# Kernel optimization log

Measured on AMD Instinct MI355X. Metric: run time of the kernel, lower is better.

The kernel has to match this reference:

```python
import jax, jax.numpy as jnp
import numpy as np

B, T, E, V, H = 2, 2048, 1024, 2048, 8
KD, HD = E // H, V // H  # key_dim=128, head_dim=256
EPS = 1e-6


def rotate_every_two(x):
    x1 = x[..., ::2]
    x2 = x[..., 1::2]
    return jnp.stack((-x2, x1), axis=-1).reshape(x.shape)


def theta_shift(x, sin, cos):
    return x * cos + rotate_every_two(x) * sin


def setup_inputs() -> dict:
    key = jax.random.key(0)
    ks = jax.random.split(key, 8)
    x = jax.random.normal(ks[0], (B, T, E), dtype=jnp.float32)
    angle = jnp.arange(T, dtype=jnp.float32)[:, None] * (1.0 / (10000.0 ** (jnp.repeat(jnp.arange(KD // 2, dtype=jnp.float32), 2) * 2.0 / KD)))
    sin = jnp.sin(angle)  # [T, KD]
    cos = jnp.cos(angle)
    # RetNet per-head causal decay mask: decay_h = 1 - 2^(-5-h)
    decay = 1.0 - 2.0 ** (-5.0 - jnp.arange(H, dtype=jnp.float32))  # [H]
    idx = jnp.arange(T, dtype=jnp.float32)
    diff = idx[:, None] - idx[None, :]  # n - m
    causal = diff >= 0
    mask = jnp.where(causal[None], jnp.exp(jnp.where(causal, diff, 0.0)[None] * jnp.log(decay)[:, None, None]), 0.0)  # [H,T,T]
    g = 2 ** (-2.5)
    Wq = jax.random.normal(ks[1], (E, E), dtype=jnp.float32) * (g * np.sqrt(2.0 / (E + E)))
    Wk = jax.random.normal(ks[2], (E, E), dtype=jnp.float32) * (g * np.sqrt(2.0 / (E + E)))
    Wv = jax.random.normal(ks[3], (E, V), dtype=jnp.float32) * (g * np.sqrt(2.0 / (E + V)))
    Wg = jax.random.normal(ks[4], (E, V), dtype=jnp.float32) * (g * np.sqrt(2.0 / (E + V)))
    Wo = jax.random.normal(ks[5], (V, E), dtype=jnp.float32) * np.sqrt(2.0 / (V + E))
    return {"x": x, "sin": sin, "cos": cos, "mask": mask,
            "Wq": Wq, "Wk": Wk, "Wv": Wv, "Wg": Wg, "Wo": Wo}


def reference(x, sin, cos, mask, Wq, Wk, Wv, Wg, Wo):
    b, t, _ = x.shape
    scaling = KD ** -0.5
    q = (x @ Wq).reshape(b, t, H, KD).transpose(0, 2, 1, 3)  # [B,H,T,KD]
    k = (x @ Wk * scaling).reshape(b, t, H, KD).transpose(0, 2, 1, 3)
    v = x @ Wv  # [B,T,V]
    g = x @ Wg
    qr = theta_shift(q, sin, cos)
    kr = theta_shift(k, sin, cos)
    vr = v.reshape(b, t, H, HD).transpose(0, 2, 1, 3)  # [B,H,T,HD]
    qk = jnp.einsum('bhsk,bhtk->bhst', qr, kr) * mask  # [B,H,T,T]
    denom = jnp.clip(jnp.abs(jax.lax.stop_gradient(qk).sum(-1, keepdims=True)), 1.0, None)
    qk = qk / denom
    out = jnp.einsum('bhst,bhtd->bhsd', qk, vr)  # [B,H,T,HD]
    out = out.transpose(0, 2, 1, 3)  # [B,T,H,HD]
    # RMSNorm over head_dim, no affine
    out = out * jax.lax.rsqrt(jnp.mean(out * out, axis=-1, keepdims=True) + EPS)
    out = out.reshape(b, t, H * HD)
    out = jax.nn.silu(g) * out
    return out @ Wo  # [B,T,E]
```

## Files before the change

kernel.cpp:

```cpp
#include <hip/hip_runtime.h>
#include <hip/hip_bf16.h>


#define B_ 2
#define T_ 2048
#define E_ 1024
#define V_ 2048
#define H_ 8
#define KD_ 128
#define HD_ 256
#define M_ 4096

typedef __attribute__((ext_vector_type(8))) short bf16x8;
typedef __attribute__((ext_vector_type(4))) float f32x4;

__device__ __forceinline__ float u2f(unsigned short u) {
    return __uint_as_float(((unsigned)u) << 16);
}
__device__ __forceinline__ unsigned short f2bu(float f) {
    unsigned x = __float_as_uint(f);
    return (unsigned short)((x + 0x7fffu + ((x >> 16) & 1u)) >> 16);
}

typedef const __attribute__((address_space(1))) void gas_t;
typedef __attribute__((address_space(3))) void las_t;
__device__ __forceinline__ void gl_lds16(const void* g, void* l) {
    __builtin_amdgcn_global_load_lds((gas_t*)g, (las_t*)l, 16, 0, 0);
}

__device__ __forceinline__ void stc(float* p, float f) { *p = f; }
__device__ __forceinline__ void stc(unsigned short* p, float f) { *p = f2bu(f); }

__global__ __launch_bounds__(256) void conv_x_kernel(
    const float* __restrict__ x, unsigned short* __restrict__ xb)
{
    const size_t i = ((size_t)blockIdx.x * 256 + threadIdx.x) * 8;
    float4 a = *(const float4*)(x + i);
    float4 c = *(const float4*)(x + i + 4);
    *(ushort4*)(xb + i)     = make_ushort4(f2bu(a.x), f2bu(a.y), f2bu(a.z), f2bu(a.w));
    *(ushort4*)(xb + i + 4) = make_ushort4(f2bu(c.x), f2bu(c.y), f2bu(c.z), f2bu(c.w));
}

__global__ __launch_bounds__(256) void transW4_kernel(
    const float* __restrict__ Wq, const float* __restrict__ Wk,
    const float* __restrict__ Wv, const float* __restrict__ Wg,
    unsigned short* __restrict__ Wt)
{
    const int z = blockIdx.z;
    const float* W; int N; int rofs;
    if (z == 0)      { W = Wq; N = 1024; rofs = 0; }
    else if (z == 1) { W = Wk; N = 1024; rofs = 1024; }
    else if (z == 2) { W = Wv; N = 2048; rofs = 2048; }
    else             { W = Wg; N = 2048; rofs = 4096; }
    const int n0 = blockIdx.x * 64;
    if (n0 >= N) return;
    const int k0 = blockIdx.y * 64;

    __shared__ float tl[64][65];
    const int tid = threadIdx.x;
    #pragma unroll
    for (int i = 0; i < 4; ++i) {
        int kr = i * 16 + (tid >> 4);
        int nc = (tid & 15) * 4;
        float4 v = *(const float4*)(W + (size_t)(k0 + kr) * N + n0 + nc);
        tl[kr][nc] = v.x; tl[kr][nc + 1] = v.y; tl[kr][nc + 2] = v.z; tl[kr][nc + 3] = v.w;
    }
    __syncthreads();
    #pragma unroll
    for (int i = 0; i < 4; ++i) {
        int nr = i * 16 + (tid >> 4);
        int kc = (tid & 15) * 4;
        ushort4 u = make_ushort4(f2bu(tl[kc + 0][nr]), f2bu(tl[kc + 1][nr]),
                                 f2bu(tl[kc + 2][nr]), f2bu(tl[kc + 3][nr]));
        *(ushort4*)(Wt + (size_t)(rofs + n0 + nr) * E_ + k0 + kc) = u;
    }
}

__global__ __launch_bounds__(256) void transW_kernel(
    const float* __restrict__ W, unsigned short* __restrict__ Wt, int K, int N)
{
    __shared__ float tl[64][65];
    const int tid = threadIdx.x;
    const int n0 = blockIdx.x * 64, k0 = blockIdx.y * 64;
    #pragma unroll
    for (int i = 0; i < 4; ++i) {
        int kr = i * 16 + (tid >> 4);
        int nc = (tid & 15) * 4;
        float4 v = *(const float4*)(W + (size_t)(k0 + kr) * N + n0 + nc);
        tl[kr][nc] = v.x; tl[kr][nc + 1] = v.y; tl[kr][nc + 2] = v.z; tl[kr][nc + 3] = v.w;
    }
    __syncthreads();
    #pragma unroll
    for (int i = 0; i < 4; ++i) {
        int nr = i * 16 + (tid >> 4);
        int kc = (tid & 15) * 4;
        ushort4 u = make_ushort4(f2bu(tl[kc + 0][nr]), f2bu(tl[kc + 1][nr]),
                                 f2bu(tl[kc + 2][nr]), f2bu(tl[kc + 3][nr]));
        *(ushort4*)(Wt + (size_t)(n0 + nr) * K + k0 + kc) = u;
    }
}

__global__ __launch_bounds__(256) void transV_kernel(
    const unsigned short* __restrict__ vb, unsigned short* __restrict__ vt)
{
    __shared__ unsigned short tl[64][68];
    const int tid = threadIdx.x;
    const int t0 = blockIdx.x * 64, c0 = blockIdx.y * 64, b = blockIdx.z;
    #pragma unroll
    for (int i = 0; i < 4; ++i) {
        int tr = i * 16 + (tid >> 4);
        int cc = (tid & 15) * 4;
        ushort4 v = *(const ushort4*)(vb + (size_t)(b * T_ + t0 + tr) * V_ + c0 + cc);
        tl[tr][cc] = v.x; tl[tr][cc + 1] = v.y; tl[tr][cc + 2] = v.z; tl[tr][cc + 3] = v.w;
    }
    __syncthreads();
    #pragma unroll
    for (int i = 0; i < 4; ++i) {
        int cr = i * 16 + (tid >> 4);
        int tc = (tid & 15) * 4;
        ushort4 u = make_ushort4(tl[tc + 0][cr], tl[tc + 1][cr], tl[tc + 2][cr], tl[tc + 3][cr]);
        *(ushort4*)(vt + (size_t)(b * V_ + c0 + cr) * T_ + t0 + tc) = u;
    }
}

#define GSTAGE(BUF, K0)                                                        \
    {                                                                          \
        _Pragma("unroll")                                                      \
        for (int i = 0; i < 4; ++i) {                                          \
            int r = i * 32 + srow;                                             \
            int cb = scolb ^ ((r & 7) << 4);                                   \
            gl_lds16((const char*)(A  + (size_t)(rowBase + r) * K + (K0)) + cb,\
                     Asm[BUF] + i * 4096 + w * 1024);                          \
            gl_lds16((const char*)(Bt + (size_t)(colBase + r) * K + (K0)) + cb,\
                     Bsm[BUF] + i * 4096 + w * 1024);                          \
        }                                                                      \
    }

#define GCOMPUTE(BUF)                                                          \
    {                                                                          \
        _Pragma("unroll")                                                      \
        for (int kk = 0; kk < 2; ++kk) {                                       \
            const int cb = kk * 64 + (l >> 4) * 16;                            \
            bf16x8 a[4], b[4];                                                 \
            _Pragma("unroll")                                                  \
            for (int m = 0; m < 4; ++m) {                                      \
                int r = wr * 64 + m * 16 + (l & 15);                           \
                a[m] = *(const bf16x8*)(Asm[BUF] + r * 128 + (cb ^ ((r & 7) << 4))); \
            }                                                                  \
            _Pragma("unroll")                                                  \
            for (int n = 0; n < 4; ++n) {                                      \
                int r = wc * 64 + n * 16 + (l & 15);                           \
                b[n] = *(const bf16x8*)(Bsm[BUF] + r * 128 + (cb ^ ((r & 7) << 4))); \
            }                                                                  \
            _Pragma("unroll")                                                  \
            for (int m = 0; m < 4; ++m)                                        \
                _Pragma("unroll")                                              \
                for (int n = 0; n < 4; ++n)                                    \
                    acc[m][n] = __builtin_amdgcn_mfma_f32_16x16x32_bf16(a[m], b[n], acc[m][n], 0, 0, 0); \
        }                                                                      \
    }

#define GEMM_PIPELINE_LOOP                                                     \
    GSTAGE(0, 0)                                                               \
    const int nk = K / 64;                                                     \
    for (int kt = 0; kt < nk; ++kt) {                                          \
        const int cur = kt & 1;                                                \
        if (kt + 1 < nk) {                                                     \
            GSTAGE(1 - cur, (kt + 1) * 64)                                     \
            asm volatile("s_waitcnt vmcnt(8)" ::: "memory");                   \
        } else {                                                               \
            asm volatile("s_waitcnt vmcnt(0)" ::: "memory");                   \
        }                                                                      \
        __builtin_amdgcn_s_barrier();                                          \
        __builtin_amdgcn_sched_barrier(0);                                     \
        GCOMPUTE(cur)                                                          \
        __builtin_amdgcn_s_barrier();                                          \
        __builtin_amdgcn_sched_barrier(0);                                     \
    }

template <typename CT>
__global__ __launch_bounds__(256) void gemm_mfma_kernel(
    const unsigned short* __restrict__ A,
    const unsigned short* __restrict__ Bt,
    CT* __restrict__ C,
    int N, int K)
{
    __shared__ __align__(16) char Asm[2][128 * 64 * 2];
    __shared__ __align__(16) char Bsm[2][128 * 64 * 2];
    const int tid = threadIdx.x;
    const int l = tid & 63;
    const int w = tid >> 6;
    const int wr = w >> 1, wc = w & 1;
    const int rowBase = blockIdx.y * 128;
    const int colBase = blockIdx.x * 128;
    const int srow = tid >> 3;
    const int scolb = (tid & 7) * 16;

    f32x4 acc[4][4] = {};

    GEMM_PIPELINE_LOOP

    #pragma unroll
    for (int m = 0; m < 4; ++m)
        #pragma unroll
        for (int n = 0; n < 4; ++n)
            #pragma unroll
            for (int r = 0; r < 4; ++r) {
                int row = rowBase + wr * 64 + m * 16 + (l >> 4) * 4 + r;
                int col = colBase + wc * 64 + n * 16 + (l & 15);
                float f = acc[m][n][r];
                if (!isfinite(f)) f = 0.f;
                stc(C + (size_t)row * N + col, f);
            }
}

__global__ __launch_bounds__(256) void gemm_qkvg_kernel(
    const unsigned short* __restrict__ A,
    const unsigned short* __restrict__ Bt,
    unsigned short* __restrict__ qb,
    unsigned short* __restrict__ kb,
    unsigned short* __restrict__ vb,
    unsigned short* __restrict__ gb)
{
    const int K = E_;
    __shared__ __align__(16) char Asm[2][128 * 64 * 2];
    __shared__ __align__(16) char Bsm[2][128 * 64 * 2];
    const int tid = threadIdx.x;
    const int l = tid & 63;
    const int w = tid >> 6;
    const int wr = w >> 1, wc = w & 1;
    const int rowBase = blockIdx.y * 128;
    const int colBase = blockIdx.x * 128;
    const int srow = tid >> 3;
    const int scolb = (tid & 7) * 16;

    f32x4 acc[4][4] = {};

    GEMM_PIPELINE_LOOP

    const int colW = colBase + wc * 64;
    unsigned short* dst;
    int cofs, stride;
    if (colW < 1024)      { dst = qb; cofs = 0;    stride = E_; }
    else if (colW < 2048) { dst = kb; cofs = 1024; stride = E_; }
    else if (colW < 4096) { dst = vb; cofs = 2048; stride = V_; }
    else                  { dst = gb; cofs = 4096; stride = V_; }
    #pragma unroll
    for (int m = 0; m < 4; ++m)
        #pragma unroll
        for (int n = 0; n < 4; ++n)
            #pragma unroll
            for (int r = 0; r < 4; ++r) {
                int row = rowBase + wr * 64 + m * 16 + (l >> 4) * 4 + r;
                int col = colW + n * 16 + (l & 15);
                float f = acc[m][n][r];
                if (!isfinite(f)) f = 0.f;
                dst[(size_t)row * stride + (col - cofs)] = f2bu(f);
            }
}

__global__ __launch_bounds__(256) void theta2_kernel(
    unsigned short* __restrict__ qb,
    unsigned short* __restrict__ kb,
    const float* __restrict__ sinp, const float* __restrict__ cosp)
{
    unsigned short* qk = blockIdx.y ? kb : qb;
    const float scale = blockIdx.y ? 0.088388347648318447f : 1.0f;
    const int i = blockIdx.x * 256 + threadIdx.x;
    const int pe = i & (E_ / 2 - 1);
    const int bt = i >> 9;
    const int t = bt & (T_ - 1);
    const int e0 = pe << 1;
    const int d0 = e0 & (KD_ - 1);
    const size_t base = (size_t)bt * E_ + e0;
    const float q0 = u2f(qk[base]);
    const float q1 = u2f(qk[base + 1]);
    const int sb = t * KD_ + d0;
    const float s0 = sinp[sb], s1 = sinp[sb + 1];
    const float c0 = cosp[sb], c1 = cosp[sb + 1];
    qk[base]     = f2bu((q0 * c0 - q1 * s0) * scale);
    qk[base + 1] = f2bu((q1 * c1 + q0 * s1) * scale);
}

#define STAGE_K(BUF, T0)                                                       \
    {                                                                          \
        _Pragma("unroll")                                                      \
        for (int i = 0; i < 4; ++i) {                                          \
            int r = i * 16 + (tid >> 4);                                       \
            int cb = ((tid & 15) * 16) ^ ((r & 7) << 4);                       \
            gl_lds16((const char*)(kb + (size_t)(b * T_ + (T0) + r) * E_ + h * KD_) + cb, \
                     Ks[BUF] + i * 4096 + w * 1024);                           \
        }                                                                      \
    }

#define STAGE_V(T0)                                                            \
    {                                                                          \
        _Pragma("unroll")                                                      \
        for (int i = 0; i < 8; ++i) {                                          \
            int r = i * 32 + (tid >> 3);                                       \
            int cb = ((tid & 7) * 16) ^ ((r & 7) << 4);                        \
            gl_lds16((const char*)(vt + (size_t)((b * H_ + h) * HD_ + r) * T_ + (T0)) + cb, \
                     Vs + i * 4096 + w * 1024);                                \
        }                                                                      \
    }

__global__ __launch_bounds__(256) void retention_mfma_kernel(
    const unsigned short* __restrict__ qb,
    const unsigned short* __restrict__ kb,
    const unsigned short* __restrict__ vt,
    unsigned short* __restrict__ ao)
{
    __shared__ __align__(16) char Ks[2][64 * 128 * 2];
    __shared__ __align__(16) char Vs[256 * 64 * 2];
    __shared__ __align__(16) char Ps[64 * 64 * 2];
    __shared__ float rsum_lds[64];
    const int tid = threadIdx.x;
    const int l = tid & 63;
    const int w = tid >> 6;
    const int orig = (int)blockIdx.x;
    const int xcd  = orig & 7;
    const int pos  = orig >> 3;
    const int slot = pos >> 5;
    const int cu   = pos & 31;
    const int half = cu >> 4;
    const int c15  = cu & 15;
    const int bh   = xcd * 2 + half;
    const int chunk = slot ? c15 : (31 - c15);
    const int b = bh >> 3, h = bh & 7;
    const int s0 = chunk * 64;
    const float ld = logf(1.f - exp2f(-5.f - (float)h));

    float es[4], etl[4];
    #pragma unroll
    for (int r = 0; r < 4; ++r)
        es[r] = __expf((float)(s0 + w * 16 + (l >> 4) * 4 + r) * ld);
    #pragma unroll
    for (int n = 0; n < 4; ++n)
        etl[n] = __expf(-(float)(n * 16 + (l & 15)) * ld);
    const float Dm64 = __expf(-64.f * ld);
    float etb = 1.f;

    bf16x8 qf[4];
    {
        const char* qp = (const char*)(qb + (size_t)(b * T_ + s0 + w * 16 + (l & 15)) * E_ + h * KD_);
        #pragma unroll
        for (int kk = 0; kk < 4; ++kk)
            qf[kk] = *(const bf16x8*)(qp + kk * 64 + (l >> 4) * 16);
    }

    f32x4 oacc[4][4] = {};
    float rs[4] = {0.f, 0.f, 0.f, 0.f};

    const int nt = chunk + 1;
    STAGE_K(0, 0)

    for (int t = 0; t < nt; ++t) {
        const int cur = t & 1;
        const int t0 = t * 64;
        STAGE_V(t0)
        if (t + 1 < nt) {
            STAGE_K(1 - cur, t0 + 64)
            asm volatile("s_waitcnt vmcnt(12)" ::: "memory");
        } else {
            asm volatile("s_waitcnt vmcnt(8)" ::: "memory");
        }
        __builtin_amdgcn_s_barrier();
        __builtin_amdgcn_sched_barrier(0);

        f32x4 sacc[4] = {};
        #pragma unroll
        for (int kk = 0; kk < 4; ++kk) {
            const int cb = kk * 64 + (l >> 4) * 16;
            #pragma unroll
            for (int n = 0; n < 4; ++n) {
                int r = n * 16 + (l & 15);
                bf16x8 kf = *(const bf16x8*)(Ks[cur] + r * 256 + (cb ^ ((r & 7) << 4)));
                sacc[n] = __builtin_amdgcn_mfma_f32_16x16x32_bf16(qf[kk], kf, sacc[n], 0, 0, 0);
            }
        }
        float et[4];
        #pragma unroll
        for (int n = 0; n < 4; ++n) et[n] = etb * etl[n];
        etb *= Dm64;
        float rsp[4] = {0.f, 0.f, 0.f, 0.f};
        #pragma unroll
        for (int n = 0; n < 4; ++n)
            #pragma unroll
            for (int r = 0; r < 4; ++r) {
                int qrow = w * 16 + (l >> 4) * 4 + r;
                int tcol = n * 16 + (l & 15);
                int d = (s0 + qrow) - (t0 + tcol);
                float pm = (d >= 0) ? sacc[n][r] * (es[r] * et[n]) : 0.f;
                rsp[r] += pm;
                *(unsigned short*)(Ps + qrow * 128 + ((tcol * 2) ^ ((qrow & 7) << 4))) = f2bu(pm);
            }
        #pragma unroll
        for (int r = 0; r < 4; ++r) {
            float vv = rsp[r];
            vv += __shfl_xor(vv, 1, 16);
            vv += __shfl_xor(vv, 2, 16);
            vv += __shfl_xor(vv, 4, 16);
            vv += __shfl_xor(vv, 8, 16);
            rs[r] += vv;
        }
        if (t + 1 < nt) {
            asm volatile("s_waitcnt vmcnt(4) lgkmcnt(0)" ::: "memory");
        } else {
            asm volatile("s_waitcnt vmcnt(0) lgkmcnt(0)" ::: "memory");
        }
        __builtin_amdgcn_s_barrier();
        __builtin_amdgcn_sched_barrier(0);
        #pragma unroll
        for (int kk = 0; kk < 2; ++kk) {
            const int cb = kk * 64 + (l >> 4) * 16;
            bf16x8 pf[4];
            #pragma unroll
            for (int m = 0; m < 4; ++m) {
                int pr = m * 16 + (l & 15);
                pf[m] = *(const bf16x8*)(Ps + pr * 128 + (cb ^ ((pr & 7) << 4)));
            }
            #pragma unroll
            for (int n = 0; n < 4; ++n) {
                int r = w * 64 + n * 16 + (l & 15);
                bf16x8 vf = *(const bf16x8*)(Vs + r * 128 + (cb ^ ((r & 7) << 4)));
                #pragma unroll
                for (int m = 0; m < 4; ++m)
                    oacc[m][n] = __builtin_amdgcn_mfma_f32_16x16x32_bf16(pf[m], vf, oacc[m][n], 0, 0, 0);
            }
        }
        __builtin_amdgcn_s_barrier();
        __builtin_amdgcn_sched_barrier(0);
    }

    #pragma unroll
    for (int r = 0; r < 4; ++r)
        if ((l & 15) == 0) rsum_lds[w * 16 + (l >> 4) * 4 + r] = rs[r];
    __syncthreads();

    #pragma unroll
    for (int m = 0; m < 4; ++m)
        #pragma unroll
        for (int r = 0; r < 4; ++r) {
            const int row = m * 16 + (l >> 4) * 4 + r;
            const float inv = 1.f / fmaxf(fabsf(rsum_lds[row]), 1.f);
            #pragma unroll
            for (int n = 0; n < 4; ++n) {
                int col = h * HD_ + w * 64 + n * 16 + (l & 15);
                float f = oacc[m][n][r] * inv;
                if (!isfinite(f)) f = 0.f;
                ao[(size_t)(b * T_ + s0 + row) * V_ + col] = f2bu(f);
            }
        }
}

__global__ __launch_bounds__(256) void rms_silu_kernel(
    unsigned short* __restrict__ ao, const unsigned short* __restrict__ g)
{
    __shared__ float part[4];
    const int tid = threadIdx.x;
    const size_t base = (size_t)blockIdx.x * HD_;
    const float f = u2f(ao[base + tid]);
    float sq = f * f;
    #pragma unroll
    for (int off = 32; off > 0; off >>= 1) sq += __shfl_down(sq, off, 64);
    if ((tid & 63) == 0) part[tid >> 6] = sq;
    __syncthreads();
    const float tot = part[0] + part[1] + part[2] + part[3];
    const float scale = rsqrtf(tot * (1.0f / HD_) + 1e-6f);
    const float gv = u2f(g[base + tid]);
    ao[base + tid] = f2bu(f * scale * gv / (1.f + __expf(-gv)));
}

extern "C" void kernel_launch(void* const* d_in, const int* in_sizes, int n_in,
                              void* d_out, int out_size, void* d_ws, size_t ws_size,
                              hipStream_t stream)
{
    const float* x    = (const float*)d_in[0];
    const float* sinp = (const float*)d_in[1];
    const float* cosp = (const float*)d_in[2];
    const float* Wq   = (const float*)d_in[4];
    const float* Wk   = (const float*)d_in[5];
    const float* Wv   = (const float*)d_in[6];
    const float* Wg   = (const float*)d_in[7];
    const float* Wo   = (const float*)d_in[8];
    float* out = (float*)d_out;

    unsigned short* xb = (unsigned short*)d_out;
    unsigned short* qb = xb + (size_t)M_ * E_;

    char* ws = (char*)d_ws;
    unsigned short* kb  = (unsigned short*)(ws + 0);
    unsigned short* vb  = (unsigned short*)(ws + 8388608);
    unsigned short* gb  = (unsigned short*)(ws + 25165824);
    unsigned short* wt  = (unsigned short*)(ws + 41943040);
    unsigned short* vt  = (unsigned short*)(ws + 54525952);
    unsigned short* aob = (unsigned short*)(ws + 71303168);
    unsigned short* wot = (unsigned short*)(ws + 88080384);

    dim3 blk(256);
    conv_x_kernel<<<M_ * E_ / 8 / 256, blk, 0, stream>>>(x, xb);

    transW4_kernel<<<dim3(32, 16, 4), blk, 0, stream>>>(Wq, Wk, Wv, Wg, wt);

    gemm_qkvg_kernel<<<dim3(48, 32), blk, 0, stream>>>(xb, wt, qb, kb, vb, gb);

    theta2_kernel<<<dim3(M_ * E_ / 2 / 256, 2), blk, 0, stream>>>(qb, kb, sinp, cosp);

    transV_kernel<<<dim3(32, 32, B_), blk, 0, stream>>>(vb, vt);

    retention_mfma_kernel<<<dim3(512), blk, 0, stream>>>(qb, kb, vt, aob);

    rms_silu_kernel<<<B_ * T_ * H_, blk, 0, stream>>>(aob, gb);

    transW_kernel<<<dim3(16, 32), blk, 0, stream>>>(Wo, wot, V_, E_);
    gemm_mfma_kernel<float><<<dim3(8, 32), blk, 0, stream>>>(aob, wot, out, E_, V_);
}
```

Baseline: 219.8 us.

## Fuse RMSNorm and SiLU gating into retention epilogue; retile output GEMM

The per-row RMSNorm over head_dim and the SiLU(g) gating are moved into the retention kernel epilogue. The squared sums are reduced across lanes and waves through LDS, so the separate rms_silu kernel and its read-modify-write of the attention output are gone. The output projection GEMM becomes a dedicated 64x128 tile kernel with twice as many blocks, to fill more CUs on a 4096x1024 output. In exchange the retention epilogue does extra global loads of g and an extra sync, and the smaller GEMM tiles reuse less data.

```diff
diff --git a/kernel.cpp b/kernel.cpp
--- a/kernel.cpp
+++ b/kernel.cpp
@@ -27,9 +27,6 @@
 __device__ __forceinline__ void gl_lds16(const void* g, void* l) {
     __builtin_amdgcn_global_load_lds((gas_t*)g, (las_t*)l, 16, 0, 0);
 }
-
-__device__ __forceinline__ void stc(float* p, float f) { *p = f; }
-__device__ __forceinline__ void stc(unsigned short* p, float f) { *p = f2bu(f); }
 
 __global__ __launch_bounds__(256) void conv_x_kernel(
     const float* __restrict__ x, unsigned short* __restrict__ xb)
@@ -178,42 +175,6 @@
         __builtin_amdgcn_sched_barrier(0);                                     \
     }
 
-template <typename CT>
-__global__ __launch_bounds__(256) void gemm_mfma_kernel(
-    const unsigned short* __restrict__ A,
-    const unsigned short* __restrict__ Bt,
-    CT* __restrict__ C,
-    int N, int K)
-{
-    __shared__ __align__(16) char Asm[2][128 * 64 * 2];
-    __shared__ __align__(16) char Bsm[2][128 * 64 * 2];
-    const int tid = threadIdx.x;
-    const int l = tid & 63;
-    const int w = tid >> 6;
-    const int wr = w >> 1, wc = w & 1;
-    const int rowBase = blockIdx.y * 128;
-    const int colBase = blockIdx.x * 128;
-    const int srow = tid >> 3;
-    const int scolb = (tid & 7) * 16;
-
-    f32x4 acc[4][4] = {};
-
-    GEMM_PIPELINE_LOOP
-
-    #pragma unroll
-    for (int m = 0; m < 4; ++m)
-        #pragma unroll
-        for (int n = 0; n < 4; ++n)
-            #pragma unroll
-            for (int r = 0; r < 4; ++r) {
-                int row = rowBase + wr * 64 + m * 16 + (l >> 4) * 4 + r;
-                int col = colBase + wc * 64 + n * 16 + (l & 15);
-                float f = acc[m][n][r];
-                if (!isfinite(f)) f = 0.f;
-                stc(C + (size_t)row * N + col, f);
-            }
-}
-
 __global__ __launch_bounds__(256) void gemm_qkvg_kernel(
     const unsigned short* __restrict__ A,
     const unsigned short* __restrict__ Bt,
@@ -256,6 +217,94 @@
                 float f = acc[m][n][r];
                 if (!isfinite(f)) f = 0.f;
                 dst[(size_t)row * stride + (col - cofs)] = f2bu(f);
+            }
+}
+
+__global__ __launch_bounds__(256) void gemm_wo_kernel(
+    const unsigned short* __restrict__ A,
+    const unsigned short* __restrict__ Bt,
+    float* __restrict__ C)
+{
+    const int K = V_;
+    __shared__ __align__(16) char Asm[2][64 * 128];
+    __shared__ __align__(16) char Bsm[2][128 * 128];
+    const int tid = threadIdx.x;
+    const int l = tid & 63;
+    const int w = tid >> 6;
+    const int wr = w >> 1, wc = w & 1;
+    const int rowBase = blockIdx.y * 64;
+    const int colBase = blockIdx.x * 128;
+    const int srow = tid >> 3;
+    const int scolb = (tid & 7) * 16;
+
+    f32x4 acc[2][4] = {};
+
+#define WSTAGE(BUF, K0)                                                        \
+    {                                                                          \
+        _Pragma("unroll")                                                      \
+        for (int i = 0; i < 2; ++i) {                                          \
+            int r = i * 32 + srow;                                             \
+            int cb = scolb ^ ((r & 7) << 4);                                   \
+            gl_lds16((const char*)(A + (size_t)(rowBase + r) * K + (K0)) + cb, \
+                     Asm[BUF] + i * 4096 + w * 1024);                          \
+        }                                                                      \
+        _Pragma("unroll")                                                      \
+        for (int i = 0; i < 4; ++i) {                                          \
+            int r = i * 32 + srow;                                             \
+            int cb = scolb ^ ((r & 7) << 4);                                   \
+            gl_lds16((const char*)(Bt + (size_t)(colBase + r) * K + (K0)) + cb,\
+                     Bsm[BUF] + i * 4096 + w * 1024);                          \
+        }                                                                      \
+    }
+
+    WSTAGE(0, 0)
+    const int nk = K / 64;
+    for (int kt = 0; kt < nk; ++kt) {
+        const int cur = kt & 1;
+        if (kt + 1 < nk) {
+            WSTAGE(1 - cur, (kt + 1) * 64)
+            asm volatile("s_waitcnt vmcnt(6)" ::: "memory");
+        } else {
+            asm volatile("s_waitcnt vmcnt(0)" ::: "memory");
+        }
+        __builtin_amdgcn_s_barrier();
+        __builtin_amdgcn_sched_barrier(0);
+        #pragma unroll
+        for (int kk = 0; kk < 2; ++kk) {
+            const int cb = kk * 64 + (l >> 4) * 16;
+            bf16x8 a[2], b[4];
+            #pragma unroll
+            for (int m = 0; m < 2; ++m) {
+                int r = wr * 32 + m * 16 + (l & 15);
+                a[m] = *(const bf16x8*)(Asm[cur] + r * 128 + (cb ^ ((r & 7) << 4)));
+            }
+            #pragma unroll
+            for (int n = 0; n < 4; ++n) {
+                int r = wc * 64 + n * 16 + (l & 15);
+                b[n] = *(const bf16x8*)(Bsm[cur] + r * 128 + (cb ^ ((r & 7) << 4)));
+            }
+            #pragma unroll
+            for (int m = 0; m < 2; ++m)
+                #pragma unroll
+                for (int n = 0; n < 4; ++n)
+                    acc[m][n] = __builtin_amdgcn_mfma_f32_16x16x32_bf16(a[m], b[n], acc[m][n], 0, 0, 0);
+        }
+        __builtin_amdgcn_s_barrier();
+        __builtin_amdgcn_sched_barrier(0);
+    }
+#undef WSTAGE
+
+    #pragma unroll
+    for (int m = 0; m < 2; ++m)
+        #pragma unroll
+        for (int n = 0; n < 4; ++n)
+            #pragma unroll
+            for (int r = 0; r < 4; ++r) {
+                int row = rowBase + wr * 32 + m * 16 + (l >> 4) * 4 + r;
+                int col = colBase + wc * 64 + n * 16 + (l & 15);
+                float f = acc[m][n][r];
+                if (!isfinite(f)) f = 0.f;
+                C[(size_t)row * E_ + col] = f;
             }
 }
 
@@ -308,12 +357,14 @@
     const unsigned short* __restrict__ qb,
     const unsigned short* __restrict__ kb,
     const unsigned short* __restrict__ vt,
+    const unsigned short* __restrict__ g,
     unsigned short* __restrict__ ao)
 {
     __shared__ __align__(16) char Ks[2][64 * 128 * 2];
     __shared__ __align__(16) char Vs[256 * 64 * 2];
     __shared__ __align__(16) char Ps[64 * 64 * 2];
     __shared__ float rsum_lds[64];
+    __shared__ float rsq_lds[4][64];
     const int tid = threadIdx.x;
     const int l = tid & 63;
     const int w = tid >> 6;
@@ -443,32 +494,38 @@
         for (int r = 0; r < 4; ++r) {
             const int row = m * 16 + (l >> 4) * 4 + r;
             const float inv = 1.f / fmaxf(fabsf(rsum_lds[row]), 1.f);
+            float ps = 0.f;
             #pragma unroll
             for (int n = 0; n < 4; ++n) {
-                int col = h * HD_ + w * 64 + n * 16 + (l & 15);
-                float f = oacc[m][n][r] * inv;
+                float o = oacc[m][n][r] * inv;
+                ps += o * o;
+            }
+            ps += __shfl_xor(ps, 1, 16);
+            ps += __shfl_xor(ps, 2, 16);
+            ps += __shfl_xor(ps, 4, 16);
+            ps += __shfl_xor(ps, 8, 16);
+            if ((l & 15) == 0) rsq_lds[w][row] = ps;
+        }
+    __syncthreads();
+
+    #pragma unroll
+    for (int m = 0; m < 4; ++m)
+        #pragma unroll
+        for (int r = 0; r < 4; ++r) {
+            const int row = m * 16 + (l >> 4) * 4 + r;
+            const float inv = 1.f / fmaxf(fabsf(rsum_lds[row]), 1.f);
+            const float tot = rsq_lds[0][row] + rsq_lds[1][row] + rsq_lds[2][row] + rsq_lds[3][row];
+            const float scale = rsqrtf(tot * (1.0f / HD_) + 1e-6f) * inv;
+            #pragma unroll
+            for (int n = 0; n < 4; ++n) {
+                const int col = h * HD_ + w * 64 + n * 16 + (l & 15);
+                const float gv = u2f(g[(size_t)(b * T_ + s0 + row) * V_ + col]);
+                const float silu = gv / (1.f + __expf(-gv));
+                float f = oacc[m][n][r] * scale * silu;
                 if (!isfinite(f)) f = 0.f;
                 ao[(size_t)(b * T_ + s0 + row) * V_ + col] = f2bu(f);
             }
         }
-}
-
-__global__ __launch_bounds__(256) void rms_silu_kernel(
-    unsigned short* __restrict__ ao, const unsigned short* __restrict__ g)
-{
-    __shared__ float part[4];
-    const int tid = threadIdx.x;
-    const size_t base = (size_t)blockIdx.x * HD_;
-    const float f = u2f(ao[base + tid]);
-    float sq = f * f;
-    #pragma unroll
-    for (int off = 32; off > 0; off >>= 1) sq += __shfl_down(sq, off, 64);
-    if ((tid & 63) == 0) part[tid >> 6] = sq;
-    __syncthreads();
-    const float tot = part[0] + part[1] + part[2] + part[3];
-    const float scale = rsqrtf(tot * (1.0f / HD_) + 1e-6f);
-    const float gv = u2f(g[base + tid]);
-    ao[base + tid] = f2bu(f * scale * gv / (1.f + __expf(-gv)));
 }
 
 extern "C" void kernel_launch(void* const* d_in, const int* in_sizes, int n_in,
@@ -508,10 +565,8 @@
 
     transV_kernel<<<dim3(32, 32, B_), blk, 0, stream>>>(vb, vt);
 
-    retention_mfma_kernel<<<dim3(512), blk, 0, stream>>>(qb, kb, vt, aob);
-
-    rms_silu_kernel<<<B_ * T_ * H_, blk, 0, stream>>>(aob, gb);
+    retention_mfma_kernel<<<dim3(512), blk, 0, stream>>>(qb, kb, vt, gb, aob);
 
     transW_kernel<<<dim3(16, 32), blk, 0, stream>>>(Wo, wot, V_, E_);
-    gemm_mfma_kernel<float><<<dim3(8, 32), blk, 0, stream>>>(aob, wot, out, E_, V_);
-}
+    gemm_wo_kernel<<<dim3(8, 64), blk, 0, stream>>>(aob, wot, out);
+}
```

Result: faster. 203.3 us (-7.5%).
